# Kernel optimization log

Measured on AMD Instinct MI355X. Metric: run time of the kernel, lower is better.

The kernel has to match this reference:

```python
import jax, jax.numpy as jnp
import numpy as np
import itertools

KH = KW = 3
N_NZ = 5
K_OUT = 126  # C(9,5) -> all patterns, matches capped n_kernels
C_IN = 128


def setup_inputs() -> dict:
    key = jax.random.key(0)
    k1, k2 = jax.random.split(key)
    inputs = jax.random.normal(k1, (32, 112, 112, C_IN), dtype=jnp.float32)
    # sparse_kernel: (n_non_zero, in_channels, kernels), glorot-ish scale
    scale = (2.0 / (N_NZ * C_IN + K_OUT)) ** 0.5
    sparse_kernel = jax.random.normal(k2, (N_NZ, C_IN, K_OUT), dtype=jnp.float32) * scale
    bias = jnp.zeros((K_OUT,), dtype=jnp.float32)
    # deterministic unique sparsity patterns: all C(9,5) flat-position combos
    patterns = jnp.asarray(
        np.array(list(itertools.combinations(range(KH * KW), N_NZ)), dtype=np.int32)
    )  # (K_OUT, N_NZ) flat positions in [0, 9)
    return {"inputs": inputs, "sparse_kernel": sparse_kernel, "bias": bias, "patterns": patterns}


def reference(inputs, sparse_kernel, bias, patterns):
    k_out = patterns.shape[0]
    c_in = sparse_kernel.shape[1]
    kk = jnp.arange(k_out)[:, None]  # (K,1) broadcasts against (K,N)
    # scatter: dense_flat[pos, :, k] = sparse_kernel[n, :, k]
    updates = jnp.transpose(sparse_kernel, (2, 0, 1))  # (K, N, Cin)
    dense_flat = jnp.zeros((KH * KW, c_in, k_out), dtype=inputs.dtype)
    dense_flat = dense_flat.at[patterns, :, kk].set(updates)
    dense_kernel = dense_flat.reshape(KH, KW, c_in, k_out)
    out = jax.lax.conv_general_dilated(
        inputs, dense_kernel, window_strides=(1, 1), padding="SAME",
        dimension_numbers=("NHWC", "HWIO", "NHWC"))
    return jax.nn.relu(out + bias)
```

## Files before the change

kernel.cpp:

```cpp
#include <hip/hip_runtime.h>
#include <hip/hip_bf16.h>


typedef __attribute__((ext_vector_type(8))) __bf16 bf16x8;
typedef __attribute__((ext_vector_type(4))) float f32x4;

__device__ __forceinline__ unsigned short f2bf(float f) {
  unsigned int u = __builtin_bit_cast(unsigned int, f);
  u += 0x7fffu + ((u >> 16) & 1u);
  return (unsigned short)(u >> 16);
}

__global__ __launch_bounds__(256) void build_B(const float* __restrict__ sk,
                                               const int* __restrict__ patterns,
                                               unsigned short* __restrict__ Bws) {
  int idx = blockIdx.x * 256 + threadIdx.x;
  if (idx >= 9 * 128 * 128) return;
  int c = idx & 127;
  int n = (idx >> 7) & 127;
  int p = idx >> 14;
  float v = 0.f;
  if (n < 126) {
#pragma unroll
    for (int j = 0; j < 5; ++j)
      if (patterns[n * 5 + j] == p) v = sk[(j * 128 + c) * 126 + n];
  }
  int cc = c >> 5, cl = c & 31;
  Bws[(((p * 4 + cc) * 128) + n) * 32 + cl] = f2bf(v);
}

__global__ __launch_bounds__(256, 2) void conv_main(const float* __restrict__ in,
                                                    const unsigned short* __restrict__ Bws,
                                                    const float* __restrict__ bias,
                                                    float* __restrict__ out) {
  __shared__ unsigned short Alds[3 * 114 * 40];

  const int tid = threadIdx.x;
  const int bid = blockIdx.x;
  const int nimg = bid / 112;
  const int y = bid - nimg * 112;
  const int lane = tid & 63;
  const int w = tid >> 6;
  const int quad = lane >> 4;
  const int lrow = lane & 15;

  const float* inb = in + (size_t)nimg * 112 * 112 * 128;

  f32x4 acc[7][2];
#pragma unroll
  for (int mt = 0; mt < 7; ++mt) { acc[mt][0] = (f32x4)0.f; acc[mt][1] = (f32x4)0.f; }

  float4 pf[11];
  auto loadA = [&](int cc) {
#pragma unroll
    for (int it = 0; it < 11; ++it) {
      int i = tid + it * 256;
      float4 v = make_float4(0.f, 0.f, 0.f, 0.f);
      if (i < 2736) {
        int c4 = i & 7;
        int rest = i >> 3;
        int r = rest / 114;
        int hx = rest - r * 114;
        int gy = y + r - 1;
        int gx = hx - 1;
        if ((unsigned)gy < 112u && (unsigned)gx < 112u)
          v = *(const float4*)(inb + ((size_t)gy * 112 + gx) * 128 + cc * 32 + c4 * 4);
      }
      pf[it] = v;
    }
  };
  auto writeA = [&]() {
#pragma unroll
    for (int it = 0; it < 11; ++it) {
      int i = tid + it * 256;
      if (i < 2736) {
        int c4 = i & 7;
        int rest = i >> 3;
        int r = rest / 114;
        int hx = rest - r * 114;
        ushort4 s;
        s.x = f2bf(pf[it].x); s.y = f2bf(pf[it].y);
        s.z = f2bf(pf[it].z); s.w = f2bf(pf[it].w);
        *(ushort4*)&Alds[(r * 114 + hx) * 40 + c4 * 4] = s;
      }
    }
  };

  loadA(0);
  writeA();
  __syncthreads();

#pragma unroll 1
  for (int cc = 0; cc < 4; ++cc) {
    bf16x8 b[9][2];
#pragma unroll
    for (int p = 0; p < 9; ++p)
#pragma unroll
      for (int j = 0; j < 2; ++j)
        b[p][j] = *(const bf16x8*)(Bws +
            (((size_t)(p * 4 + cc) * 128 + w * 32 + j * 16 + lrow) * 32 + quad * 8));

    if (cc < 3) loadA(cc + 1);

#pragma unroll
    for (int p = 0; p < 9; ++p) {
      const int r = p / 3;
      const int px = p - r * 3;
      const int abase = (r * 114 + px + lrow) * 40 + quad * 8;
#pragma unroll
      for (int mt = 0; mt < 7; ++mt) {
        bf16x8 a = *(const bf16x8*)&Alds[abase + mt * 16 * 40];
        acc[mt][0] = __builtin_amdgcn_mfma_f32_16x16x32_bf16(a, b[p][0], acc[mt][0], 0, 0, 0);
        acc[mt][1] = __builtin_amdgcn_mfma_f32_16x16x32_bf16(a, b[p][1], acc[mt][1], 0, 0, 0);
      }
    }

    if (cc < 3) {
      __syncthreads();
      writeA();
      __syncthreads();
    }
  }

  const int k0 = w * 32 + lrow;
  const int k1 = k0 + 16;
  const float bv0 = bias[k0 < 126 ? k0 : 125];
  const float bv1 = bias[k1 < 126 ? k1 : 125];
  float* outrow = out + ((size_t)(nimg * 112 + y)) * 112 * 126;
#pragma unroll
  for (int mt = 0; mt < 7; ++mt) {
#pragma unroll
    for (int rg = 0; rg < 4; ++rg) {
      int x = mt * 16 + quad * 4 + rg;
      float* o = outrow + (size_t)x * 126;
      if (k0 < 126) { float v = acc[mt][0][rg] + bv0; o[k0] = v > 0.f ? v : 0.f; }
      if (k1 < 126) { float v = acc[mt][1][rg] + bv1; o[k1] = v > 0.f ? v : 0.f; }
    }
  }
}

extern "C" void kernel_launch(void* const* d_in, const int* in_sizes, int n_in,
                              void* d_out, int out_size, void* d_ws, size_t ws_size,
                              hipStream_t stream) {
  const float* in = (const float*)d_in[0];
  const float* sk = (const float*)d_in[1];
  const float* bias = (const float*)d_in[2];
  const int* patterns = (const int*)d_in[3];
  float* out = (float*)d_out;
  unsigned short* Bws = (unsigned short*)d_ws;

  build_B<<<dim3(576), dim3(256), 0, stream>>>(sk, patterns, Bws);
  conv_main<<<dim3(32 * 112), dim3(256), 0, stream>>>(in, Bws, bias, out);
}
```

Before: 434.0 us.

## Compute two output rows per block with double-buffered LDS and streamed B

Each block now produces two output rows instead of one. Warps are split by row and by a 64-wide output-channel half, so each input halo row staged in LDS feeds both rows, which reduces redundant global reads of the input. The A tile is double-buffered and its next-chunk load and convert are split into two halves interleaved with the MFMA loop, which removes the mid-loop barrier pair. B fragments are loaded per tap with one-ahead prefetch instead of all nine up front, cutting register pressure. The cost is a 28-accumulator register tile, twice the LDS per block and half as many blocks, which may hurt occupancy.

```diff
diff --git a/kernel.cpp b/kernel.cpp
--- a/kernel.cpp
+++ b/kernel.cpp
@@ -33,108 +33,123 @@
                                                     const unsigned short* __restrict__ Bws,
                                                     const float* __restrict__ bias,
                                                     float* __restrict__ out) {
-  __shared__ unsigned short Alds[3 * 114 * 40];
+  __shared__ unsigned short Alds[2][4 * 114 * 40];
 
   const int tid = threadIdx.x;
   const int bid = blockIdx.x;
-  const int nimg = bid / 112;
-  const int y = bid - nimg * 112;
+  const int nimg = bid / 56;
+  const int y0 = (bid - nimg * 56) * 2;
   const int lane = tid & 63;
   const int w = tid >> 6;
+  const int r = w >> 1;
+  const int nh = w & 1;
   const int quad = lane >> 4;
   const int lrow = lane & 15;
 
   const float* inb = in + (size_t)nimg * 112 * 112 * 128;
 
-  f32x4 acc[7][2];
+  f32x4 acc[7][4];
 #pragma unroll
-  for (int mt = 0; mt < 7; ++mt) { acc[mt][0] = (f32x4)0.f; acc[mt][1] = (f32x4)0.f; }
+  for (int mt = 0; mt < 7; ++mt)
+#pragma unroll
+    for (int jf = 0; jf < 4; ++jf) acc[mt][jf] = (f32x4)0.f;
 
-  float4 pf[11];
-  auto loadA = [&](int cc) {
+  float4 pf[8];
+  auto loadA = [&](int cc, int hh) {
 #pragma unroll
-    for (int it = 0; it < 11; ++it) {
+    for (int it = 0; it < 8; ++it) {
       int i = tid + it * 256;
       float4 v = make_float4(0.f, 0.f, 0.f, 0.f);
-      if (i < 2736) {
-        int c4 = i & 7;
-        int rest = i >> 3;
-        int r = rest / 114;
-        int hx = rest - r * 114;
-        int gy = y + r - 1;
+      if (i < 1824) {
+        int c4 = i & 3;
+        int rest = i >> 2;
+        int hr = rest / 114;
+        int hx = rest - hr * 114;
+        int gy = y0 + hr - 1;
         int gx = hx - 1;
         if ((unsigned)gy < 112u && (unsigned)gx < 112u)
-          v = *(const float4*)(inb + ((size_t)gy * 112 + gx) * 128 + cc * 32 + c4 * 4);
+          v = *(const float4*)(inb + ((size_t)gy * 112 + gx) * 128 + cc * 32 + hh * 16 + c4 * 4);
       }
       pf[it] = v;
     }
   };
-  auto writeA = [&]() {
+  auto writeA = [&](int buf, int hh) {
 #pragma unroll
-    for (int it = 0; it < 11; ++it) {
+    for (int it = 0; it < 8; ++it) {
       int i = tid + it * 256;
-      if (i < 2736) {
-        int c4 = i & 7;
-        int rest = i >> 3;
-        int r = rest / 114;
-        int hx = rest - r * 114;
+      if (i < 1824) {
+        int c4 = i & 3;
+        int rest = i >> 2;
+        int hr = rest / 114;
+        int hx = rest - hr * 114;
         ushort4 s;
         s.x = f2bf(pf[it].x); s.y = f2bf(pf[it].y);
         s.z = f2bf(pf[it].z); s.w = f2bf(pf[it].w);
-        *(ushort4*)&Alds[(r * 114 + hx) * 40 + c4 * 4] = s;
+        *(ushort4*)&Alds[buf][(hr * 114 + hx) * 40 + hh * 16 + c4 * 4] = s;
       }
     }
   };
 
-  loadA(0);
-  writeA();
+  auto bload = [&](int cc, int p, bf16x8* b) {
+#pragma unroll
+    for (int jf = 0; jf < 4; ++jf)
+      b[jf] = *(const bf16x8*)(Bws +
+          (((size_t)(p * 4 + cc) * 128 + nh * 64 + jf * 16 + lrow) * 32 + quad * 8));
+  };
+
+  loadA(0, 0); writeA(0, 0);
+  loadA(0, 1); writeA(0, 1);
   __syncthreads();
 
 #pragma unroll 1
   for (int cc = 0; cc < 4; ++cc) {
-    bf16x8 b[9][2];
-#pragma unroll
-    for (int p = 0; p < 9; ++p)
-#pragma unroll
-      for (int j = 0; j < 2; ++j)
-        b[p][j] = *(const bf16x8*)(Bws +
-            (((size_t)(p * 4 + cc) * 128 + w * 32 + j * 16 + lrow) * 32 + quad * 8));
-
-    if (cc < 3) loadA(cc + 1);
+    const int buf = cc & 1;
+    bf16x8 bcur[4], bnxt[4];
+    bload(cc, 0, bcur);
+    if (cc < 3) loadA(cc + 1, 0);
 
 #pragma unroll
     for (int p = 0; p < 9; ++p) {
-      const int r = p / 3;
-      const int px = p - r * 3;
-      const int abase = (r * 114 + px + lrow) * 40 + quad * 8;
+      if (p < 8) bload(cc, p + 1, bnxt);
+      const int dy = p / 3;
+      const int px = p - dy * 3;
+      const int abase = ((r + dy) * 114 + px + lrow) * 40 + quad * 8;
 #pragma unroll
       for (int mt = 0; mt < 7; ++mt) {
-        bf16x8 a = *(const bf16x8*)&Alds[abase + mt * 16 * 40];
-        acc[mt][0] = __builtin_amdgcn_mfma_f32_16x16x32_bf16(a, b[p][0], acc[mt][0], 0, 0, 0);
-        acc[mt][1] = __builtin_amdgcn_mfma_f32_16x16x32_bf16(a, b[p][1], acc[mt][1], 0, 0, 0);
+        bf16x8 a = *(const bf16x8*)&Alds[buf][abase + mt * 16 * 40];
+        acc[mt][0] = __builtin_amdgcn_mfma_f32_16x16x32_bf16(a, bcur[0], acc[mt][0], 0, 0, 0);
+        acc[mt][1] = __builtin_amdgcn_mfma_f32_16x16x32_bf16(a, bcur[1], acc[mt][1], 0, 0, 0);
+        acc[mt][2] = __builtin_amdgcn_mfma_f32_16x16x32_bf16(a, bcur[2], acc[mt][2], 0, 0, 0);
+        acc[mt][3] = __builtin_amdgcn_mfma_f32_16x16x32_bf16(a, bcur[3], acc[mt][3], 0, 0, 0);
+      }
+      if (p < 8) {
+#pragma unroll
+        for (int jf = 0; jf < 4; ++jf) bcur[jf] = bnxt[jf];
+      }
+      if (cc < 3 && p == 4) {
+        writeA(buf ^ 1, 0);
+        loadA(cc + 1, 1);
       }
     }
-
-    if (cc < 3) {
-      __syncthreads();
-      writeA();
-      __syncthreads();
-    }
+    if (cc < 3) writeA(buf ^ 1, 1);
+    __syncthreads();
   }
 
-  const int k0 = w * 32 + lrow;
-  const int k1 = k0 + 16;
-  const float bv0 = bias[k0 < 126 ? k0 : 125];
-  const float bv1 = bias[k1 < 126 ? k1 : 125];
-  float* outrow = out + ((size_t)(nimg * 112 + y)) * 112 * 126;
+  float* outrow = out + ((size_t)(nimg * 112 + y0 + r)) * 112 * 126;
 #pragma unroll
-  for (int mt = 0; mt < 7; ++mt) {
+  for (int jf = 0; jf < 4; ++jf) {
+    const int k = nh * 64 + jf * 16 + lrow;
+    if (k < 126) {
+      const float bv = bias[k];
 #pragma unroll
-    for (int rg = 0; rg < 4; ++rg) {
-      int x = mt * 16 + quad * 4 + rg;
-      float* o = outrow + (size_t)x * 126;
-      if (k0 < 126) { float v = acc[mt][0][rg] + bv0; o[k0] = v > 0.f ? v : 0.f; }
-      if (k1 < 126) { float v = acc[mt][1][rg] + bv1; o[k1] = v > 0.f ? v : 0.f; }
+      for (int mt = 0; mt < 7; ++mt) {
+#pragma unroll
+        for (int rg = 0; rg < 4; ++rg) {
+          int x = mt * 16 + quad * 4 + rg;
+          float v = acc[mt][jf][rg] + bv;
+          outrow[(size_t)x * 126 + k] = v > 0.f ? v : 0.f;
+        }
+      }
     }
   }
 }
@@ -150,5 +165,5 @@
   unsigned short* Bws = (unsigned short*)d_ws;
 
   build_B<<<dim3(576), dim3(256), 0, stream>>>(sk, patterns, Bws);
-  conv_main<<<dim3(32 * 112), dim3(256), 0, stream>>>(in, Bws, bias, out);
+  conv_main<<<dim3(32 * 56), dim3(256), 0, stream>>>(in, Bws, bias, out);
 }
```

Result: slower. 532.0 us (+22.6%).
